# Performance work log

Hardware: AMD Instinct MI355X
Metric: run time of the kernel (lower is better)

Reference implementation:

```python
import jax, jax.numpy as jnp
import numpy as np

B, D, T, NT, DS, G = 1024, 512, 36, 64, 32, 4
EPS = 1e-5


def setup_inputs() -> dict:
    key = jax.random.key(0)
    ks = jax.random.split(key, 8)
    return {
        "x": jax.random.normal(ks[0], (B, D, T, 1), jnp.float32),
        "y": jax.random.normal(ks[1], (B, D, T, 1), jnp.float32),
        "my_tokens": jax.random.normal(ks[2], (NT, D), jnp.float32) * 0.02,
        "gate": jax.random.normal(ks[3], (1,), jnp.float32) * 0.1,
        "gate_av": jax.random.normal(ks[4], (1,), jnp.float32) * 0.1,
        "w_down": jax.random.normal(ks[5], (DS, D // G), jnp.float32) * 0.05,  # Conv2d(512->32,1,groups=4) weight [32,128,1,1] squeezed
        "w_up": jax.random.normal(ks[6], (D, DS // G), jnp.float32) * 0.05,    # Conv2d(32->512,1,groups=4) weight [512,8,1,1] squeezed
        "bn1_g": jnp.ones((DS,), jnp.float32), "bn1_b": jnp.zeros((DS,), jnp.float32),
        "bn2_g": jnp.ones((D,), jnp.float32), "bn2_b": jnp.zeros((D,), jnp.float32),
        "lnb_g": jnp.ones((D,), jnp.float32), "lnb_b": jnp.zeros((D,), jnp.float32),
        "lnp_g": jnp.ones((D,), jnp.float32), "lnp_b": jnp.zeros((D,), jnp.float32),
    }


def _layernorm(h, g, b):  # normalize last dim
    mu = jnp.mean(h, axis=-1, keepdims=True)
    var = jnp.var(h, axis=-1, keepdims=True)
    return (h - mu) * jax.lax.rsqrt(var + EPS) * g + b


def _batchnorm(z, g, b):  # z: [B,C,T], training-mode batch stats over (B,T)
    mu = jnp.mean(z, axis=(0, 2), keepdims=True)
    var = jnp.var(z, axis=(0, 2), keepdims=True)
    return (z - mu) * jax.lax.rsqrt(var + EPS) * g[None, :, None] + b[None, :, None]


def reference(x, y, my_tokens, gate, gate_av, w_down, w_up,
              bn1_g, bn1_b, bn2_g, bn2_b, lnb_g, lnb_b, lnp_g, lnp_b):
    xs = x[..., 0]  # [B,D,T]
    ys = y[..., 0]  # [B,D,T]
    # token <- y cross attention
    att_y2tk = jax.nn.softmax(jnp.einsum('td,bds->bts', my_tokens, ys), axis=-1)  # [B,NT,T]
    rep = my_tokens[None] + jnp.einsum('bts,bds->btd', att_y2tk, ys)  # [B,NT,D]
    # x <- token cross attention
    att_tk2x = jax.nn.softmax(jnp.einsum('bds,btd->bst', xs, rep), axis=-1)  # [B,T,NT]
    x_res = jnp.einsum('bst,btd->bsd', att_tk2x, rep)  # [B,T,D]
    xc = xs + gate_av[0] * jnp.swapaxes(x_res, 1, 2)  # [B,D,T]
    # ln_before over channel dim
    h = jnp.swapaxes(_layernorm(jnp.swapaxes(xc, 1, 2), lnb_g, lnb_b), 1, 2)  # [B,D,T]
    # grouped 1x1 down conv
    hg = h.reshape(h.shape[0], G, D // G, T)
    z = jnp.einsum('bgct,goc->bgot', hg, w_down.reshape(G, DS // G, D // G)).reshape(h.shape[0], DS, T)
    z = jax.nn.relu(_batchnorm(z, bn1_g, bn1_b))
    # grouped 1x1 up conv
    zg = z.reshape(z.shape[0], G, DS // G, T)
    o = jnp.einsum('bgct,goc->bgot', zg, w_up.reshape(G, D // G, DS // G)).reshape(z.shape[0], D, T)
    o = _batchnorm(o, bn2_g, bn2_b)
    o = jnp.swapaxes(_layernorm(jnp.swapaxes(o, 1, 2), lnp_g, lnp_b), 1, 2)
    return (gate[0] * o)[..., None]  # [B,D,T,1]
```

## Files before the change

### kernel.cpp

```cpp
#include <hip/hip_runtime.h>

#define B_ 1024
#define D_ 512
#define T_ 36
#define NT_ 64
#define DS_ 32
#define EPS_ 1e-5f

typedef float f32x4 __attribute__((ext_vector_type(4)));
typedef __bf16 bf16x8 __attribute__((ext_vector_type(8)));
typedef unsigned short u16x8 __attribute__((ext_vector_type(8)));
typedef unsigned short u16x4 __attribute__((ext_vector_type(4)));

#define DEVI static __device__ __forceinline__
#define MFMA16 __builtin_amdgcn_mfma_f32_16x16x32_bf16

DEVI unsigned short f2bf(float f) { return __builtin_bit_cast(unsigned short, (__bf16)f); }
DEVI float bf2f(unsigned short h) { return (float)__builtin_bit_cast(__bf16, h); }

DEVI unsigned swz(int row, int col) {
    return (unsigned)(row * 1024 + ((2 * col) ^ ((row & 7) << 4)));
}

DEVI f32x4 tile16_gl(const unsigned short* __restrict__ Arow, const char* img, int brow, int l4)
{
    bf16x8 Ar[4], Br[4];
    #pragma unroll
    for (int p = 0; p < 4; ++p) {
        int k0 = p * 32 + l4 * 8;
        Ar[p] = *(const bf16x8*)(Arow + k0);
        Br[p] = *(const bf16x8*)(img + swz(brow, k0));
    }
    f32x4 acc = {0.f, 0.f, 0.f, 0.f};
    #pragma unroll
    for (int ks = 0; ks < 16; ++ks) {
        bf16x8 a = Ar[ks & 3], bv = Br[ks & 3];
        if (ks < 12) {
            int k0 = (ks + 4) * 32 + l4 * 8;
            Ar[ks & 3] = *(const bf16x8*)(Arow + k0);
            Br[ks & 3] = *(const bf16x8*)(img + swz(brow, k0));
        }
        acc = MFMA16(a, bv, acc, 0, 0, 0);
    }
    return acc;
}

DEVI f32x4 tile16_ll(const char* imgA, int arow, const char* imgB, int brow, int l4)
{
    bf16x8 Ar[4], Br[4];
    #pragma unroll
    for (int p = 0; p < 4; ++p) {
        int k0 = p * 32 + l4 * 8;
        Ar[p] = *(const bf16x8*)(imgA + swz(arow, k0));
        Br[p] = *(const bf16x8*)(imgB + swz(brow, k0));
    }
    f32x4 acc = {0.f, 0.f, 0.f, 0.f};
    #pragma unroll
    for (int ks = 0; ks < 16; ++ks) {
        bf16x8 a = Ar[ks & 3], bv = Br[ks & 3];
        if (ks < 12) {
            int k0 = (ks + 4) * 32 + l4 * 8;
            Ar[ks & 3] = *(const bf16x8*)(imgA + swz(arow, k0));
            Br[ks & 3] = *(const bf16x8*)(imgB + swz(brow, k0));
        }
        acc = MFMA16(a, bv, acc, 0, 0, 0);
    }
    return acc;
}

#define OFF_XST 73728
#define OFF_SC  122880
#define OFF_A1  133632
#define OFF_A2  142848
#define OFF_GT  149760
#define K1_LDS  156672

__global__ __launch_bounds__(512)
void k0_prepack(const float* __restrict__ tok, const float* __restrict__ wd,
                unsigned short* __restrict__ tokbf, float* __restrict__ tokTf,
                unsigned short* __restrict__ wdd)
{
    int i = blockIdx.x * 512 + threadIdx.x;
    if (i < 32768) {
        tokbf[i] = f2bf(tok[i]);
    } else if (i < 65536) {
        int j = i - 32768; int d = j >> 6, t = j & 63;
        tokTf[j] = tok[t * 512 + d];
    } else if (i < 81920) {
        int j = i - 65536; int o = j >> 9, dd = j & 511;
        wdd[j] = ((dd >> 7) == (o >> 3)) ? f2bf(wd[o * 128 + (dd & 127)]) : (unsigned short)0;
    }
}

__global__ __launch_bounds__(1024, 4)
void k1_fused(const float* __restrict__ x, const float* __restrict__ y,
              const unsigned short* __restrict__ tokbf, const float* __restrict__ tokTf,
              const float* __restrict__ gav_p, const unsigned short* __restrict__ wdd,
              const float* __restrict__ lnbg, const float* __restrict__ lnbb,
              float* __restrict__ z_pre)
{
    extern __shared__ char lds[];
    float* sc = (float*)(lds + OFF_SC);
    unsigned short* a1 = (unsigned short*)(lds + OFF_A1);
    unsigned short* a2 = (unsigned short*)(lds + OFF_A2);
    unsigned short* gt = (unsigned short*)(lds + OFF_GT);

    const int b    = blockIdx.x;
    const int tid  = threadIdx.x;
    const int lane = tid & 63;
    const int w    = tid >> 6;
    const int l15  = lane & 15;
    const int l4   = lane >> 4;

    const float* yb = y + b * (D_ * T_);
    const float* xb = x + b * (D_ * T_);

    {
        unsigned* z1 = (unsigned*)(lds + 36 * 1024);
        unsigned* z2 = (unsigned*)(lds + OFF_XST + 36 * 1024);
        for (int i = tid; i < 3072; i += 1024) { z1[i] = 0u; z2[i] = 0u; }
        unsigned* z3 = (unsigned*)(lds + OFF_A1);
        for (int i = tid; i < 5760; i += 1024) z3[i] = 0u;
    }
    for (int ww = tid; ww < 1152; ww += 1024) {
        int isx = (ww >= 576) ? 1 : 0;
        int u = isx ? (ww - 576) : ww;
        const float* src = isx ? xb : yb;
        char* dst = lds + (isx ? OFF_XST : 0);
        int dblk = u / 9, s4 = u - dblk * 9;
        int s0 = s4 * 4;
        const float* bp = src + dblk * 8 * T_ + s0;
        u16x8 u0, u1, u2, u3;
        #pragma unroll
        for (int r = 0; r < 8; ++r) {
            f32x4 v = *(const f32x4*)(bp + r * T_);
            u0[r] = f2bf(v[0]); u1[r] = f2bf(v[1]);
            u2[r] = f2bf(v[2]); u3[r] = f2bf(v[3]);
        }
        *(u16x8*)(dst + swz(s0 + 0, dblk * 8)) = u0;
        *(u16x8*)(dst + swz(s0 + 1, dblk * 8)) = u1;
        *(u16x8*)(dst + swz(s0 + 2, dblk * 8)) = u2;
        *(u16x8*)(dst + swz(s0 + 3, dblk * 8)) = u3;
    }
    __syncthreads();

    for (int tile = w; tile < 21; tile += 16) {
        if (tile < 12) {
            int mt = tile / 3, nt = tile % 3;
            int trow = mt * 16 + l15, srow = nt * 16 + l15;
            f32x4 acc = tile16_gl(tokbf + trow * 512, lds, srow, l4);
            if (srow < T_) {
                #pragma unroll
                for (int j = 0; j < 4; ++j)
                    sc[(mt * 16 + l4 * 4 + j) * 42 + srow] = acc[j];
            }
        } else {
            int g2 = tile - 12;
            int mt = g2 / 3, nt = g2 % 3;
            int arow = mt * 16 + l15, brow = nt * 16 + l15;
            f32x4 acc = tile16_ll(lds + OFF_XST, arow, lds, brow, l4);
            #pragma unroll
            for (int j = 0; j < 4; ++j) {
                int gr = mt * 16 + l4 * 4 + j;
                if (gr < T_) gt[gr * 72 + brow] = f2bf(acc[j]);
            }
        }
    }
    __syncthreads();

    {
        int t = tid >> 4, l16 = tid & 15;
        const float* scp = sc + t * 42;
        float v0 = scp[l16];
        float v1 = scp[l16 + 16];
        float v2 = (l16 < 4) ? scp[l16 + 32] : -1e30f;
        float m = fmaxf(fmaxf(v0, v1), v2);
        #pragma unroll
        for (int off = 1; off < 16; off <<= 1) m = fmaxf(m, __shfl_xor(m, off));
        float e0 = __expf(v0 - m), e1 = __expf(v1 - m);
        float e2 = (l16 < 4) ? __expf(v2 - m) : 0.f;
        float ssum = e0 + e1 + e2;
        #pragma unroll
        for (int off = 1; off < 16; off <<= 1) ssum += __shfl_xor(ssum, off);
        float inv = 1.f / ssum;
        a1[t * 72 + l16]      = f2bf(e0 * inv);
        a1[t * 72 + l16 + 16] = f2bf(e1 * inv);
        if (l16 < 4) a1[t * 72 + l16 + 32] = f2bf(e2 * inv);
    }
    for (int j = tid; j < 4608; j += 1024) {
        int row = j / 9, q = j - row * 9;
        f32x4 v = *(const f32x4*)(yb + row * T_ + q * 4);
        u16x4 hh;
        #pragma unroll
        for (int jj = 0; jj < 4; ++jj) hh[jj] = f2bf(v[jj]);
        *(u16x4*)(lds + row * 144 + q * 8) = hh;
    }
    if (tid < 512) {
        char* p = lds + tid * 144;
        u16x4 z4 = {0,0,0,0}; u16x8 z8 = {0,0,0,0,0,0,0,0};
        *(u16x4*)(p + 72) = z4;
        *(u16x8*)(p + 80) = z8;
        *(u16x8*)(p + 96) = z8;
        *(u16x8*)(p + 112) = z8;
    }
    __syncthreads();

    {
        #pragma unroll
        for (int half = 0; half < 2; ++half) {
            int dbase = (w + 16 * half) * 16;
            bf16x8 fa0 = *(const bf16x8*)(lds + (dbase + l15) * 144 + l4 * 16);
            bf16x8 fa1 = *(const bf16x8*)(lds + (dbase + l15) * 144 + 64 + l4 * 16);
            bf16x8 fb0[4], fb1[4];
            #pragma unroll
            for (int tt = 0; tt < 4; ++tt) {
                fb0[tt] = *(const bf16x8*)(a1 + (tt * 16 + l15) * 72 + l4 * 8);
                fb1[tt] = *(const bf16x8*)(a1 + (tt * 16 + l15) * 72 + 32 + l4 * 8);
            }
            float tv[16];
            #pragma unroll
            for (int tt = 0; tt < 4; ++tt)
                #pragma unroll
                for (int j = 0; j < 4; ++j)
                    tv[tt * 4 + j] = tokTf[(dbase + l4 * 4 + j) * 64 + tt * 16 + l15];
            f32x4 c[4];
            #pragma unroll
            for (int tt = 0; tt < 4; ++tt) {
                f32x4 acc = {0.f,0.f,0.f,0.f};
                acc = MFMA16(fa0, fb0[tt], acc, 0, 0, 0);
                acc = MFMA16(fa1, fb1[tt], acc, 0, 0, 0);
                c[tt] = acc;
            }
            #pragma unroll
            for (int tt = 0; tt < 4; ++tt) {
                #pragma unroll
                for (int j = 0; j < 4; ++j) {
                    int d = dbase + l4 * 4 + j;
                    *(unsigned short*)(lds + d * 144 + 2 * (tt * 16 + l15)) =
                        f2bf(tv[tt * 4 + j] + c[tt][j]);
                }
            }
        }
    }
    if (w < 12) {
        int mt = w / 3, nt = w % 3;
        int trow = mt * 16 + l15, srow = nt * 16 + l15;
        bf16x8 sa0 = *(const bf16x8*)(a1 + trow * 72 + l4 * 8);
        bf16x8 sa1 = *(const bf16x8*)(a1 + trow * 72 + 32 + l4 * 8);
        bf16x8 sb0 = *(const bf16x8*)(gt + srow * 72 + l4 * 8);
        bf16x8 sb1 = *(const bf16x8*)(gt + srow * 72 + 32 + l4 * 8);
        f32x4 acc = tile16_gl(tokbf + trow * 512, lds + OFF_XST, srow, l4);
        acc = MFMA16(sa0, sb0, acc, 0, 0, 0);
        acc = MFMA16(sa1, sb1, acc, 0, 0, 0);
        if (srow < T_) {
            #pragma unroll
            for (int j = 0; j < 4; ++j)
                sc[(mt * 16 + l4 * 4 + j) * 42 + srow] = acc[j];
        }
    }
    __syncthreads();

    if (tid < 576) {
        int s = tid >> 4, l16 = tid & 15;
        float v0 = sc[(l16     ) * 42 + s];
        float v1 = sc[(l16 + 16) * 42 + s];
        float v2 = sc[(l16 + 32) * 42 + s];
        float v3 = sc[(l16 + 48) * 42 + s];
        float m = fmaxf(fmaxf(v0, v1), fmaxf(v2, v3));
        #pragma unroll
        for (int off = 1; off < 16; off <<= 1) m = fmaxf(m, __shfl_xor(m, off));
        float e0 = __expf(v0 - m), e1 = __expf(v1 - m), e2 = __expf(v2 - m), e3 = __expf(v3 - m);
        float ssum = e0 + e1 + e2 + e3;
        #pragma unroll
        for (int off = 1; off < 16; off <<= 1) ssum += __shfl_xor(ssum, off);
        float inv = 1.f / ssum;
        a2[s * 72 + l16]      = f2bf(e0 * inv);
        a2[s * 72 + l16 + 16] = f2bf(e1 * inv);
        a2[s * 72 + l16 + 32] = f2bf(e2 * inv);
        a2[s * 72 + l16 + 48] = f2bf(e3 * inv);
    }
    __syncthreads();

    {
        const float gav = gav_p[0];
        float* red = sc;
        f32x4 acc6[6];
        bf16x8 pa[2][2], pb[2][2];
        {
            int q0 = w * 6;
            int dbase = (q0 & 31) * 16, sbase = (q0 >> 5) * 16;
            #pragma unroll
            for (int ks = 0; ks < 2; ++ks) {
                pa[0][ks] = *(const bf16x8*)(lds + (dbase + l15) * 144 + (ks * 32 + l4 * 8) * 2);
                pb[0][ks] = *(const bf16x8*)(a2 + (sbase + l15) * 72 + ks * 32 + l4 * 8);
            }
        }
        #pragma unroll
        for (int i = 0; i < 6; ++i) {
            int cur = i & 1, nxt = cur ^ 1;
            if (i < 5) {
                int q = w * 6 + i + 1;
                int dbase = (q & 31) * 16, sbase = (q >> 5) * 16;
                #pragma unroll
                for (int ks = 0; ks < 2; ++ks) {
                    pa[nxt][ks] = *(const bf16x8*)(lds + (dbase + l15) * 144 + (ks * 32 + l4 * 8) * 2);
                    pb[nxt][ks] = *(const bf16x8*)(a2 + (sbase + l15) * 72 + ks * 32 + l4 * 8);
                }
            }
            f32x4 acc = {0.f,0.f,0.f,0.f};
            acc = MFMA16(pa[cur][0], pb[cur][0], acc, 0, 0, 0);
            acc = MFMA16(pa[cur][1], pb[cur][1], acc, 0, 0, 0);
            acc6[i] = acc;
        }
        #pragma unroll
        for (int i = 0; i < 6; ++i) {
            int q = w * 6 + i;
            int dt = q & 31, st = q >> 5;
            int dbase = dt * 16, sbase = st * 16;
            int s = sbase + l15;
            float rsum = 0.f, rsq = 0.f;
            if (s < T_) {
                #pragma unroll
                for (int j = 0; j < 4; ++j) {
                    int d = dbase + l4 * 4 + j;
                    float xsv = bf2f(*(const unsigned short*)(lds + OFF_XST + swz(s, d)));
                    float v = xsv + gav * acc6[i][j];
                    acc6[i][j] = v;
                    rsum += v; rsq += v * v;
                }
            }
            rsum += __shfl_xor(rsum, 16); rsq += __shfl_xor(rsq, 16);
            rsum += __shfl_xor(rsum, 32); rsq += __shfl_xor(rsq, 32);
            if (s < T_ && l4 == 0) {
                red[dt * 40 + s] = rsum;
                red[1280 + dt * 40 + s] = rsq;
            }
        }
        __syncthreads();
        if (tid < T_) {
            int s = tid; float S = 0.f, Q = 0.f;
            #pragma unroll
            for (int q = 0; q < 32; ++q) { S += red[q * 40 + s]; Q += red[1280 + q * 40 + s]; }
            float mu = S * (1.f / 512.f);
            float var = Q * (1.f / 512.f) - mu * mu;
            red[2560 + s] = mu; red[2600 + s] = rsqrtf(var + EPS_);
        }
        __syncthreads();
        #pragma unroll
        for (int i = 0; i < 6; ++i) {
            int q = w * 6 + i;
            int dt = q & 31, st = q >> 5;
            int dbase = dt * 16, sbase = st * 16;
            int s = sbase + l15;
            if (s < T_) {
                float mu = red[2560 + s], rsig = red[2600 + s];
                #pragma unroll
                for (int j = 0; j < 4; ++j) {
                    int d = dbase + l4 * 4 + j;
                    float g = lnbg[d], bb2 = lnbb[d];
                    *(unsigned short*)(lds + OFF_XST + swz(s, d)) =
                        f2bf((acc6[i][j] - mu) * rsig * g + bb2);
                }
            }
        }
    }
    __syncthreads();

    if (w < 6) {
        int mt = w / 3, nt = w % 3;
        int orow = mt * 16 + l15, srow = nt * 16 + l15;
        f32x4 acc = tile16_gl(wdd + orow * 512, lds + OFF_XST, srow, l4);
        if (srow < T_) {
            #pragma unroll
            for (int j = 0; j < 4; ++j)
                z_pre[b * (DS_ * T_) + (mt * 16 + l4 * 4 + j) * T_ + srow] = acc[j];
        }
    }
}

__global__ __launch_bounds__(256)
void k3a_bn1part(const float* __restrict__ z_pre, float* __restrict__ p3)
{
    __shared__ float rbuf[4][2];
    int blk = blockIdx.x;
    int o = blk & 31, sl = blk >> 5;
    int tid = threadIdx.x;
    float S = 0.f, Q = 0.f;
    for (int i = tid; i < 64 * T_; i += 256) {
        int bb = sl * 64 + i / T_, t = i - (i / T_) * T_;
        float v = z_pre[bb * (DS_ * T_) + o * T_ + t];
        S += v; Q += v * v;
    }
    #pragma unroll
    for (int off = 1; off < 64; off <<= 1) { S += __shfl_xor(S, off); Q += __shfl_xor(Q, off); }
    int ww = tid >> 6;
    if ((tid & 63) == 0) { rbuf[ww][0] = S; rbuf[ww][1] = Q; }
    __syncthreads();
    if (tid == 0) {
        float s2 = 0.f, q2 = 0.f;
        for (int i = 0; i < 4; ++i) { s2 += rbuf[i][0]; q2 += rbuf[i][1]; }
        p3[blk * 2] = s2; p3[blk * 2 + 1] = q2;
    }
}

__global__ __launch_bounds__(64)
void k3b_bn1stats(const float* __restrict__ p3, float* __restrict__ st1)
{
    int o = threadIdx.x;
    if (o < 32) {
        float S = 0.f, Q = 0.f;
        for (int sl = 0; sl < 16; ++sl) {
            S += p3[((sl << 5) | o) * 2];
            Q += p3[((sl << 5) | o) * 2 + 1];
        }
        float mu = S / 36864.f;
        float var = Q / 36864.f - mu * mu;
        st1[o] = mu; st1[32 + o] = rsqrtf(var + EPS_);
    }
}

__global__ __launch_bounds__(256)
void k4m_moments(const float* __restrict__ z_pre, const float* __restrict__ st1,
                 const float* __restrict__ g1p, const float* __restrict__ b1p,
                 float* __restrict__ m4)
{
    __shared__ float zr[32][40];
    int blk = blockIdx.x, tid = threadIdx.x;
    int c2 = tid & 7, c1 = (tid >> 3) & 7, g = tid >> 6;
    int ch1 = g * 8 + c1, ch2 = g * 8 + c2;
    float acc = 0.f, asum = 0.f;
    for (int bi = 0; bi < 8; ++bi) {
        int b = blk * 8 + bi;
        __syncthreads();
        for (int i = tid; i < DS_ * T_; i += 256) {
            int o = i / T_, t = i - o * T_;
            float v = z_pre[b * (DS_ * T_) + i];
            zr[o][t] = fmaxf(0.f, (v - st1[o]) * st1[32 + o] * g1p[o] + b1p[o]);
        }
        __syncthreads();
        for (int t = 0; t < T_; ++t) {
            float a = zr[ch1][t], b2 = zr[ch2][t];
            acc += a * b2;
            asum += a;
        }
    }
    m4[blk * 288 + tid] = acc;
    if (c1 == c2) m4[blk * 288 + 256 + g * 8 + c1] = asum;
}

__global__ __launch_bounds__(512)
void k4s_bn2stats(const float* __restrict__ m4, const float* __restrict__ wu,
                  float* __restrict__ st2)
{
    __shared__ float M2[256], mz[32];
    int tid = threadIdx.x;
    if (tid < 256) {
        float S = 0.f;
        for (int k = 0; k < 128; ++k) S += m4[k * 288 + tid];
        M2[tid] = S * (1.f / 36864.f);
    } else if (tid < 288) {
        int j = tid - 256;
        float S = 0.f;
        for (int k = 0; k < 128; ++k) S += m4[k * 288 + 256 + j];
        mz[j] = S * (1.f / 36864.f);
    }
    __syncthreads();
    int d = tid, g = d >> 7;
    float wr[8];
    #pragma unroll
    for (int c = 0; c < 8; ++c) wr[c] = wu[d * 8 + c];
    float mu2 = 0.f;
    #pragma unroll
    for (int c = 0; c < 8; ++c) mu2 += wr[c] * mz[g * 8 + c];
    float e2 = 0.f;
    #pragma unroll
    for (int c = 0; c < 8; ++c)
        #pragma unroll
        for (int c2 = 0; c2 < 8; ++c2)
            e2 += wr[c] * wr[c2] * M2[g * 64 + c * 8 + c2];
    st2[d] = mu2;
    st2[512 + d] = rsqrtf(e2 - mu2 * mu2 + EPS_);
}

#define K5_LDS 47888
__global__ __launch_bounds__(512, 6)
void k5_final(const float* __restrict__ z_pre, const float* __restrict__ st1,
              const float* __restrict__ g1p, const float* __restrict__ b1p,
              const float* __restrict__ wu, const float* __restrict__ st2,
              const float* __restrict__ g2p, const float* __restrict__ b2p,
              const float* __restrict__ lnpg, const float* __restrict__ lnpb,
              const float* __restrict__ gate_p, float* __restrict__ out)
{
    extern __shared__ char lds[];
    unsigned short* o_f = (unsigned short*)lds;
    float* zrT = (float*)(lds + 41984);
    int b = blockIdx.x;
    int tid = threadIdx.x;

    for (int i = tid; i < DS_ * T_; i += 512) {
        int o = i / T_, s = i - o * T_;
        float v = z_pre[b * (DS_ * T_) + i];
        zrT[s * 41 + o] = fmaxf(0.f, (v - st1[o]) * st1[32 + o] * g1p[o] + b1p[o]);
    }
    __syncthreads();

    for (int i = tid; i < D_ * T_; i += 512) {
        int d = i / T_, t = i - d * T_;
        const float* zp = &zrT[t * 41 + (d >> 7) * 8];
        const float* wp = &wu[d * 8];
        f32x4 w0 = *(const f32x4*)wp;
        f32x4 w1 = *(const f32x4*)(wp + 4);
        float acc = zp[0]*w0[0] + zp[1]*w0[1] + zp[2]*w0[2] + zp[3]*w0[3]
                  + zp[4]*w1[0] + zp[5]*w1[1] + zp[6]*w1[2] + zp[7]*w1[3];
        o_f[d * 41 + t] = f2bf((acc - st2[d]) * st2[512 + d] * g2p[d] + b2p[d]);
    }
    __syncthreads();

    int w = tid >> 6, lane = tid & 63;
    float gate = gate_p[0];
    for (int t = w; t < T_; t += 8) {
        float S = 0.f, Q = 0.f;
        float v[8];
        #pragma unroll
        for (int i2 = 0; i2 < 8; ++i2) {
            float vv = bf2f(o_f[(i2 * 64 + lane) * 41 + t]);
            v[i2] = vv; S += vv; Q += vv * vv;
        }
        #pragma unroll
        for (int off = 1; off < 64; off <<= 1) { S += __shfl_xor(S, off); Q += __shfl_xor(Q, off); }
        float mu = S * (1.f / 512.f);
        float var = Q * (1.f / 512.f) - mu * mu;
        float rs = rsqrtf(var + EPS_);
        #pragma unroll
        for (int i2 = 0; i2 < 8; ++i2) {
            int d = i2 * 64 + lane;
            o_f[d * 41 + t] = f2bf(gate * ((v[i2] - mu) * rs * lnpg[d] + lnpb[d]));
        }
    }
    __syncthreads();

    float* ob = out + b * (D_ * T_);
    for (int i = tid; i < D_ * T_; i += 512) {
        int d = i / T_, t = i - d * T_;
        ob[i] = bf2f(o_f[d * 41 + t]);
    }
}

extern "C" void kernel_launch(void* const* d_in, const int* in_sizes, int n_in,
                              void* d_out, int out_size, void* d_ws, size_t ws_size,
                              hipStream_t stream)
{
    (void)in_sizes; (void)n_in; (void)out_size; (void)ws_size;
    const float* x    = (const float*)d_in[0];
    const float* y    = (const float*)d_in[1];
    const float* tok  = (const float*)d_in[2];
    const float* gate = (const float*)d_in[3];
    const float* gav  = (const float*)d_in[4];
    const float* wd   = (const float*)d_in[5];
    const float* wu   = (const float*)d_in[6];
    const float* bn1g = (const float*)d_in[7];
    const float* bn1b = (const float*)d_in[8];
    const float* bn2g = (const float*)d_in[9];
    const float* bn2b = (const float*)d_in[10];
    const float* lnbg = (const float*)d_in[11];
    const float* lnbb = (const float*)d_in[12];
    const float* lnpg = (const float*)d_in[13];
    const float* lnpb = (const float*)d_in[14];
    float* out = (float*)d_out;

    char* ws = (char*)d_ws;
    float* z_pre          = (float*)ws;
    float* st1            = (float*)(ws + 4718592);
    unsigned short* tokbf = (unsigned short*)(ws + 4719104);
    float* tokTf          = (float*)(ws + 4784640);
    unsigned short* wdd   = (unsigned short*)(ws + 4915712);
    float* p3             = (float*)(ws + 4948480);
    float* m4             = (float*)(ws + 4952576);
    float* st2            = (float*)(ws + 5100032);

    hipFuncSetAttribute((const void*)k1_fused, hipFuncAttributeMaxDynamicSharedMemorySize, K1_LDS);
    hipFuncSetAttribute((const void*)k5_final, hipFuncAttributeMaxDynamicSharedMemorySize, K5_LDS);

    k0_prepack<<<160, 512, 0, stream>>>(tok, wd, tokbf, tokTf, wdd);
    k1_fused<<<B_, 1024, K1_LDS, stream>>>(x, y, tokbf, tokTf, gav, wdd, lnbg, lnbb, z_pre);
    k3a_bn1part<<<512, 256, 0, stream>>>(z_pre, p3);
    k3b_bn1stats<<<1, 64, 0, stream>>>(p3, st1);
    k4m_moments<<<128, 256, 0, stream>>>(z_pre, st1, bn1g, bn1b, m4);
    k4s_bn2stats<<<1, 512, 0, stream>>>(m4, wu, st2);
    k5_final<<<B_, 512, K5_LDS, stream>>>(z_pre, st1, bn1g, bn1b, wu, st2, bn2g, bn2b,
                                          lnpg, lnpb, gate, out);
}
```

Measured before the change: 199.4 us.

## Vectorize LDS accesses and split MFMA accumulators in tile helpers

```diff
diff --git a/kernel.cpp b/kernel.cpp
--- a/kernel.cpp
+++ b/kernel.cpp
@@ -24,48 +24,26 @@
 
 DEVI f32x4 tile16_gl(const unsigned short* __restrict__ Arow, const char* img, int brow, int l4)
 {
-    bf16x8 Ar[4], Br[4];
+    f32x4 acc0 = {0.f,0.f,0.f,0.f}, acc1 = {0.f,0.f,0.f,0.f};
     #pragma unroll
-    for (int p = 0; p < 4; ++p) {
-        int k0 = p * 32 + l4 * 8;
-        Ar[p] = *(const bf16x8*)(Arow + k0);
-        Br[p] = *(const bf16x8*)(img + swz(brow, k0));
-    }
-    f32x4 acc = {0.f, 0.f, 0.f, 0.f};
+    for (int ks = 0; ks < 16; ks += 2) {
+        int ka = ks * 32 + l4 * 8, kb = ka + 32;
+        acc0 = MFMA16(*(const bf16x8*)(Arow + ka), *(const bf16x8*)(img + swz(brow, ka)), acc0, 0, 0, 0);
+        acc1 = MFMA16(*(const bf16x8*)(Arow + kb), *(const bf16x8*)(img + swz(brow, kb)), acc1, 0, 0, 0);
+    }
+    return acc0 + acc1;
+}
+
+DEVI f32x4 tile16_ll(const char* imgA, int arow, const char* imgB, int brow, int l4)
+{
+    f32x4 acc0 = {0.f,0.f,0.f,0.f}, acc1 = {0.f,0.f,0.f,0.f};
     #pragma unroll
-    for (int ks = 0; ks < 16; ++ks) {
-        bf16x8 a = Ar[ks & 3], bv = Br[ks & 3];
-        if (ks < 12) {
-            int k0 = (ks + 4) * 32 + l4 * 8;
-            Ar[ks & 3] = *(const bf16x8*)(Arow + k0);
-            Br[ks & 3] = *(const bf16x8*)(img + swz(brow, k0));
-        }
-        acc = MFMA16(a, bv, acc, 0, 0, 0);
-    }
-    return acc;
-}
-
-DEVI f32x4 tile16_ll(const char* imgA, int arow, const char* imgB, int brow, int l4)
-{
-    bf16x8 Ar[4], Br[4];
-    #pragma unroll
-    for (int p = 0; p < 4; ++p) {
-        int k0 = p * 32 + l4 * 8;
-        Ar[p] = *(const bf16x8*)(imgA + swz(arow, k0));
-        Br[p] = *(const bf16x8*)(imgB + swz(brow, k0));
-    }
-    f32x4 acc = {0.f, 0.f, 0.f, 0.f};
-    #pragma unroll
-    for (int ks = 0; ks < 16; ++ks) {
-        bf16x8 a = Ar[ks & 3], bv = Br[ks & 3];
-        if (ks < 12) {
-            int k0 = (ks + 4) * 32 + l4 * 8;
-            Ar[ks & 3] = *(const bf16x8*)(imgA + swz(arow, k0));
-            Br[ks & 3] = *(const bf16x8*)(imgB + swz(brow, k0));
-        }
-        acc = MFMA16(a, bv, acc, 0, 0, 0);
-    }
-    return acc;
+    for (int ks = 0; ks < 16; ks += 2) {
+        int ka = ks * 32 + l4 * 8, kb = ka + 32;
+        acc0 = MFMA16(*(const bf16x8*)(imgA + swz(arow, ka)), *(const bf16x8*)(imgB + swz(brow, ka)), acc0, 0, 0, 0);
+        acc1 = MFMA16(*(const bf16x8*)(imgA + swz(arow, kb)), *(const bf16x8*)(imgB + swz(brow, kb)), acc1, 0, 0, 0);
+    }
+    return acc0 + acc1;
 }
 
 #define OFF_XST 73728
@@ -206,39 +184,29 @@
     __syncthreads();
 
     {
-        #pragma unroll
-        for (int half = 0; half < 2; ++half) {
-            int dbase = (w + 16 * half) * 16;
-            bf16x8 fa0 = *(const bf16x8*)(lds + (dbase + l15) * 144 + l4 * 16);
-            bf16x8 fa1 = *(const bf16x8*)(lds + (dbase + l15) * 144 + 64 + l4 * 16);
-            bf16x8 fb0[4], fb1[4];
-            #pragma unroll
-            for (int tt = 0; tt < 4; ++tt) {
-                fb0[tt] = *(const bf16x8*)(a1 + (tt * 16 + l15) * 72 + l4 * 8);
-                fb1[tt] = *(const bf16x8*)(a1 + (tt * 16 + l15) * 72 + 32 + l4 * 8);
-            }
-            float tv[16];
-            #pragma unroll
-            for (int tt = 0; tt < 4; ++tt)
+        int db0 = w * 32;
+        bf16x8 Bf[2][2];
+        #pragma unroll
+        for (int n = 0; n < 2; ++n)
+            #pragma unroll
+            for (int kh = 0; kh < 2; ++kh)
+                Bf[n][kh] = *(const bf16x8*)(lds + (db0 + n * 16 + l15) * 144 + kh * 64 + l4 * 16);
+        #pragma unroll
+        for (int m = 0; m < 4; ++m) {
+            bf16x8 A0 = *(const bf16x8*)(a1 + (m * 16 + l15) * 72 + l4 * 8);
+            bf16x8 A1 = *(const bf16x8*)(a1 + (m * 16 + l15) * 72 + 32 + l4 * 8);
+            #pragma unroll
+            for (int n = 0; n < 2; ++n) {
+                f32x4 acc = {0.f,0.f,0.f,0.f};
+                acc = MFMA16(A0, Bf[n][0], acc, 0, 0, 0);
+                acc = MFMA16(A1, Bf[n][1], acc, 0, 0, 0);
+                int d = db0 + n * 16 + l15;
+                int t0 = m * 16 + l4 * 4;
+                f32x4 tv = *(const f32x4*)(tokTf + d * 64 + t0);
+                u16x4 o;
                 #pragma unroll
-                for (int j = 0; j < 4; ++j)
-                    tv[tt * 4 + j] = tokTf[(dbase + l4 * 4 + j) * 64 + tt * 16 + l15];
-            f32x4 c[4];
-            #pragma unroll
-            for (int tt = 0; tt < 4; ++tt) {
-                f32x4 acc = {0.f,0.f,0.f,0.f};
-                acc = MFMA16(fa0, fb0[tt], acc, 0, 0, 0);
-                acc = MFMA16(fa1, fb1[tt], acc, 0, 0, 0);
-                c[tt] = acc;
-            }
-            #pragma unroll
-            for (int tt = 0; tt < 4; ++tt) {
-                #pragma unroll
-                for (int j = 0; j < 4; ++j) {
-                    int d = dbase + l4 * 4 + j;
-                    *(unsigned short*)(lds + d * 144 + 2 * (tt * 16 + l15)) =
-                        f2bf(tv[tt * 4 + j] + c[tt][j]);
-                }
+                for (int j = 0; j < 4; ++j) o[j] = f2bf(tv[j] + acc[j]);
+                *(u16x4*)(lds + d * 144 + 2 * t0) = o;
             }
         }
     }
@@ -320,11 +288,10 @@
             int s = sbase + l15;
             float rsum = 0.f, rsq = 0.f;
             if (s < T_) {
+                u16x4 xv = *(const u16x4*)(lds + OFF_XST + swz(s, dbase + l4 * 4));
                 #pragma unroll
                 for (int j = 0; j < 4; ++j) {
-                    int d = dbase + l4 * 4 + j;
-                    float xsv = bf2f(*(const unsigned short*)(lds + OFF_XST + swz(s, d)));
-                    float v = xsv + gav * acc6[i][j];
+                    float v = bf2f(xv[j]) + gav * acc6[i][j];
                     acc6[i][j] = v;
                     rsum += v; rsq += v * v;
                 }
@@ -354,13 +321,13 @@
             int s = sbase + l15;
             if (s < T_) {
                 float mu = red[2560 + s], rsig = red[2600 + s];
+                f32x4 gv  = *(const f32x4*)(lnbg + dbase + l4 * 4);
+                f32x4 bv2 = *(const f32x4*)(lnbb + dbase + l4 * 4);
+                u16x4 hv;
                 #pragma unroll
-                for (int j = 0; j < 4; ++j) {
-                    int d = dbase + l4 * 4 + j;
-                    float g = lnbg[d], bb2 = lnbb[d];
-                    *(unsigned short*)(lds + OFF_XST + swz(s, d)) =
-                        f2bf((acc6[i][j] - mu) * rsig * g + bb2);
-                }
+                for (int j = 0; j < 4; ++j)
+                    hv[j] = f2bf((acc6[i][j] - mu) * rsig * gv[j] + bv2[j]);
+                *(u16x4*)(lds + OFF_XST + swz(s, dbase + l4 * 4)) = hv;
             }
         }
     }
```

New measurement: 206.1 us. +3.3%, slower.
